# Optimization experiments

Measured on AMD Instinct MI355X. Metric: run time of the kernel, lower is better.

## Reference

```python
import jax, jax.numpy as jnp
import numpy as np

B_NW, N, DIM, NH, DH, HID, NW, WH = 2048, 64, 512, 16, 32, 384, 64, 8
EPS = 1e-12  # F.normalize eps

def _rel_coords_log(wh, ww):
    # torch.cartesian_prod order: i (rows) outer, j (cols) inner
    ii, jj = np.meshgrid(np.arange(wh), np.arange(ww), indexing='ij')
    coords = np.stack([ii.ravel(), jj.ravel()], axis=-1).astype(np.float32)  # [N,2]
    rel = coords[:, None, :] - coords[None, :, :]                            # [N,N,2]
    return (np.sign(rel) * np.log1p(np.abs(rel))).astype(np.float32)

def setup_inputs() -> dict:
    key = jax.random.key(0)
    ks = jax.random.split(key, 9)
    s = 0.02
    inner = NH * DH
    return {
        'x': jax.random.normal(ks[0], (B_NW, N, DIM), jnp.float32),
        'mask': jax.random.normal(ks[1], (NW, N, N), jnp.float32),
        'w_qkv': jax.random.normal(ks[2], (DIM, 3 * inner), jnp.float32) * s,
        'tau': jnp.ones((1, NH, 1, 1), jnp.float32),
        'mlp_w1': jax.random.normal(ks[3], (2, HID), jnp.float32) * s,
        'mlp_b1': jnp.zeros((HID,), jnp.float32),
        'mlp_w2': jax.random.normal(ks[4], (HID, NH), jnp.float32) * s,
        'mlp_b2': jnp.zeros((NH,), jnp.float32),
        'w_out': jax.random.normal(ks[5], (inner, DIM), jnp.float32) * s,
        'b_out': jnp.zeros((DIM,), jnp.float32),
        'rel_log': jnp.asarray(_rel_coords_log(WH, WH)),
    }

def reference(x, mask, w_qkv, tau, mlp_w1, mlp_b1, mlp_w2, mlp_b2, w_out, b_out, rel_log):
    b, n, _ = x.shape
    qkv = x @ w_qkv                                   # [b, n, 3*nh*dh]
    qkv = qkv.reshape(b, n, 3, NH, DH)
    q, k, v = (jnp.transpose(qkv[:, :, i], (0, 2, 1, 3)) for i in range(3))  # [b, nh, n, dh]
    # cosine attention: L2-normalize q and k along head dim
    q = q / jnp.maximum(jnp.linalg.norm(q, axis=-1, keepdims=True), EPS)
    k = k / jnp.maximum(jnp.linalg.norm(k, axis=-1, keepdims=True), EPS)
    sim = jnp.einsum('bhid,bhjd->bhij', q, k) * tau   # learned temperature
    # relative position bias via meta MLP: [N,N,2] -> [N,N,nh]
    bias = jax.nn.relu(rel_log @ mlp_w1 + mlp_b1) @ mlp_w2 + mlp_b2
    sim = sim + jnp.transpose(bias, (2, 0, 1))[None]  # [1, nh, N, N]
    nw = mask.shape[0]
    sim = sim.reshape(b // nw, nw, NH, n, n) + mask[None, :, None]
    sim = sim.reshape(b, NH, n, n)
    attn = jax.nn.softmax(sim, axis=-1)
    out = jnp.einsum('bhij,bhjd->bhid', attn, v)
    out = jnp.transpose(out, (0, 2, 1, 3)).reshape(b, n, NH * DH)
    return out @ w_out + b_out
```

## Files before the change

### kernel.cpp

```cpp
#include <hip/hip_runtime.h>
#include <hip/hip_bf16.h>


typedef __bf16 bf16;
typedef __bf16 v4bf __attribute__((ext_vector_type(4)));
typedef __bf16 v8bf __attribute__((ext_vector_type(8)));
typedef float  v4f  __attribute__((ext_vector_type(4)));

__device__ __forceinline__ int swz(int o) { return o ^ (((o >> 7) & 7) << 4); }

__global__ void convert_w_kernel(const float* __restrict__ wqkv, const float* __restrict__ wout,
                                 bf16* __restrict__ Wt, bf16* __restrict__ WoT) {
    int idx = blockIdx.x * 256 + threadIdx.x;
    Wt[idx] = (bf16)wqkv[(idx & 511) * 1536 + (idx >> 9)];
    if (idx < 262144) WoT[idx] = (bf16)wout[(idx & 511) * 512 + (idx >> 9)];
}

__global__ void bias_kernel(const float* __restrict__ rel_log, const float* __restrict__ w1,
                            const float* __restrict__ b1, const float* __restrict__ w2,
                            const float* __restrict__ b2, float* __restrict__ bias) {
    int p = blockIdx.x * 256 + threadIdx.x;
    float ra = rel_log[p * 2 + 0];
    float rb = rel_log[p * 2 + 1];
    float acc[16];
    #pragma unroll
    for (int t = 0; t < 16; ++t) acc[t] = 0.f;
    for (int kk = 0; kk < 384; ++kk) {
        float hv = fmaxf(ra * w1[kk] + rb * w1[384 + kk] + b1[kk], 0.f);
        #pragma unroll
        for (int t = 0; t < 16; ++t) acc[t] += hv * w2[kk * 16 + t];
    }
    #pragma unroll
    for (int t = 0; t < 16; ++t) bias[t * 4096 + p] = acc[t] + b2[t];
}

__global__ void comb_kernel(const float* __restrict__ bias, const float* __restrict__ mask,
                            float* __restrict__ comb) {
    int idx = blockIdx.x * 256 + threadIdx.x;
    int t = idx & 4095, wh = idx >> 12;
    int w = wh >> 4, h = wh & 15;
    int ji = t >> 8, rem = t & 255;
    int j = ji >> 2, i = ji & 3;
    int q16 = rem >> 2, r = t & 3;
    int lq = q16 >> 4, lm = q16 & 15;
    int p = (i * 16 + lm) * 64 + j * 16 + lq * 4 + r;
    comb[idx] = bias[h * 4096 + p] + mask[w * 4096 + p];
}

__global__ __launch_bounds__(256) void qkv_gemm_kernel(
    const float* __restrict__ x,
    const bf16* __restrict__ Wt,
    bf16* __restrict__ q_ws, bf16* __restrict__ k_ws, bf16* __restrict__ v_ws)
{
    __shared__ alignas(16) char Alds[2][8192];
    __shared__ alignas(16) char Blds[2][8192];
    const int bid = blockIdx.x, nwg = gridDim.x;
    const int wid = (bid & 7) * (nwg >> 3) + (bid >> 3);
    const int nb = wid % 12, mb = wid / 12;

    const int t = threadIdx.x;
    const int wv = t >> 6, lane = t & 63, lq = lane >> 4, lm = lane & 15;
    const int wr = wv >> 1, wc = wv & 1;

    const int srow = t >> 1, scol = (t & 1) * 16;
    const float* aptr = x + (size_t)(mb * 128 + srow) * 512 + scol;
    const int wbyte = srow * 64 + scol * 2;
    const int wo0 = swz(wbyte), wo1 = swz(wbyte + 16);

    const char* bBase = (const char*)Wt + (size_t)(nb * 128) * 1024;
    int so[2], brow[2], bcol[2];
    #pragma unroll
    for (int p = 0; p < 2; ++p) {
        so[p] = p * 4096 + t * 16;
        int s = swz(so[p]);
        brow[p] = s >> 6; bcol[p] = s & 63;
    }
    auto stageB = [&](int buf, int kt) {
        #pragma unroll
        for (int p = 0; p < 2; ++p)
            __builtin_amdgcn_global_load_lds(
                (const __attribute__((address_space(1))) void*)(bBase + (size_t)brow[p] * 1024 + kt * 64 + bcol[p]),
                (__attribute__((address_space(3))) void*)(&Blds[buf][0] + so[p]),
                16, 0, 0);
    };
    auto writeA = [&](int buf, float4 f0, float4 f1, float4 f2, float4 f3) {
        v8bf a0 = { (bf16)f0.x, (bf16)f0.y, (bf16)f0.z, (bf16)f0.w,
                    (bf16)f1.x, (bf16)f1.y, (bf16)f1.z, (bf16)f1.w };
        v8bf a1 = { (bf16)f2.x, (bf16)f2.y, (bf16)f2.z, (bf16)f2.w,
                    (bf16)f3.x, (bf16)f3.y, (bf16)f3.z, (bf16)f3.w };
        *(v8bf*)(&Alds[buf][0] + wo0) = a0;
        *(v8bf*)(&Alds[buf][0] + wo1) = a1;
    };

    int aoff[4], boff[4];
    #pragma unroll
    for (int i = 0; i < 4; ++i) {
        aoff[i] = swz((wr * 64 + i * 16 + lm) * 64 + lq * 16);
        boff[i] = swz((wc * 64 + i * 16 + lm) * 64 + lq * 16);
    }

    v4f acc[4][4];
    #pragma unroll
    for (int i = 0; i < 4; ++i)
        #pragma unroll
        for (int j = 0; j < 4; ++j) acc[i][j] = v4f{0.f, 0.f, 0.f, 0.f};

    {
        const float4* ap = (const float4*)aptr;
        float4 f0 = ap[0], f1 = ap[1], f2 = ap[2], f3 = ap[3];
        stageB(0, 0);
        writeA(0, f0, f1, f2, f3);
        __syncthreads();
    }

    #pragma unroll 1
    for (int kt = 0; kt < 16; ++kt) {
        const int cur = kt & 1;
        float4 f0, f1, f2, f3;
        if (kt < 15) {
            const float4* ap = (const float4*)(aptr + (kt + 1) * 32);
            f0 = ap[0]; f1 = ap[1]; f2 = ap[2]; f3 = ap[3];
            stageB(cur ^ 1, kt + 1);
        }
        v8bf af[4], bfj[4];
        #pragma unroll
        for (int i = 0; i < 4; ++i) af[i] = *(const v8bf*)(&Alds[cur][0] + aoff[i]);
        #pragma unroll
        for (int j = 0; j < 4; ++j) bfj[j] = *(const v8bf*)(&Blds[cur][0] + boff[j]);
        #pragma unroll
        for (int i = 0; i < 4; ++i)
            #pragma unroll
            for (int j = 0; j < 4; ++j)
                acc[i][j] = __builtin_amdgcn_mfma_f32_16x16x32_bf16(af[i], bfj[j], acc[i][j], 0, 0, 0);
        if (kt < 15) writeA(cur ^ 1, f0, f1, f2, f3);
        __syncthreads();
    }

    const int bw = mb * 2 + wr;
    if (nb < 8) {
        bf16* dst = (nb < 4) ? q_ws : k_ws;
        const int hbase = (nb & 3) * 4 + wc * 2;
        #pragma unroll
        for (int tpair = 0; tpair < 2; ++tpair) {
            const int h = hbase + tpair;
            #pragma unroll
            for (int i = 0; i < 4; ++i)
                #pragma unroll
                for (int r = 0; r < 4; ++r) {
                    int n = i * 16 + lq * 4 + r;
                    size_t base = ((size_t)(bw * 16 + h) * 64 + n) * 32;
                    dst[base + lm]      = (bf16)acc[i][2 * tpair][r];
                    dst[base + 16 + lm] = (bf16)acc[i][2 * tpair + 1][r];
                }
        }
    } else {
        #pragma unroll
        for (int j = 0; j < 4; ++j) {
            const int h = (nb - 8) * 4 + wc * 2 + (j >> 1);
            const int dh = (j & 1) * 16 + lm;
            #pragma unroll
            for (int i = 0; i < 4; ++i) {
                v4bf pv = { (bf16)acc[i][j][0], (bf16)acc[i][j][1],
                            (bf16)acc[i][j][2], (bf16)acc[i][j][3] };
                *(v4bf*)(v_ws + ((size_t)(bw * 16 + h) * 32 + dh) * 64 + i * 16 + lq * 4) = pv;
            }
        }
    }
}

__global__ __launch_bounds__(256) void attn_kernel(
    const bf16* __restrict__ q_ws,
    const bf16* __restrict__ k_ws,
    const bf16* __restrict__ v_ws,
    const float* __restrict__ comb,
    const float* __restrict__ tau,
    int wofs,
    bf16* __restrict__ attn_out)
{
    __shared__ alignas(16) bf16 P_all[4][64 * 72];
    const int blk = blockIdx.x;
    const int b = blk >> 2, g = blk & 3;
    const int tid = threadIdx.x;
    const int wv = tid >> 6, lane = tid & 63, lq = lane >> 4, lm = lane & 15;
    const int h = g * 4 + wv;
    const v4f z4 = {0.f, 0.f, 0.f, 0.f};

    bf16* P = P_all[wv];
    const size_t qk_base = (size_t)(b * 16 + h) * 64 * 32;
    const float* comb_hw = comb + ((size_t)(((wofs + b) & 63) * 16 + h)) * 4096
                                + (lq * 16 + lm) * 4;
    const float tau_h = tau[h];

    v8bf qf[4], kf[4];
    #pragma unroll
    for (int i = 0; i < 4; ++i)
        qf[i] = *(const v8bf*)(q_ws + qk_base + (i * 16 + lm) * 32 + lq * 8);
    #pragma unroll
    for (int j = 0; j < 4; ++j)
        kf[j] = *(const v8bf*)(k_ws + qk_base + (j * 16 + lm) * 32 + lq * 8);

    #pragma unroll
    for (int i = 0; i < 4; ++i) {
        float a = 0.f;
        #pragma unroll
        for (int e = 0; e < 8; ++e) { float f = (float)qf[i][e]; a = fmaf(f, f, a); }
        a += __shfl_xor(a, 16); a += __shfl_xor(a, 32);
        float sc = tau_h / fmaxf(sqrtf(a), 1e-12f);
        #pragma unroll
        for (int e = 0; e < 8; ++e) qf[i][e] = (bf16)((float)qf[i][e] * sc);
    }
    #pragma unroll
    for (int j = 0; j < 4; ++j) {
        float a = 0.f;
        #pragma unroll
        for (int e = 0; e < 8; ++e) { float f = (float)kf[j][e]; a = fmaf(f, f, a); }
        a += __shfl_xor(a, 16); a += __shfl_xor(a, 32);
        float sc = 1.0f / fmaxf(sqrtf(a), 1e-12f);
        #pragma unroll
        for (int e = 0; e < 8; ++e) kf[j][e] = (bf16)((float)kf[j][e] * sc);
    }

    v4f st[4][4];
    #pragma unroll
    for (int j = 0; j < 4; ++j)
        #pragma unroll
        for (int i = 0; i < 4; ++i)
            st[j][i] = __builtin_amdgcn_mfma_f32_16x16x32_bf16(kf[j], qf[i], z4, 0, 0, 0);

    #pragma unroll
    for (int j = 0; j < 4; ++j)
        #pragma unroll
        for (int i = 0; i < 4; ++i) {
            float4 cv = *(const float4*)(comb_hw + (j * 4 + i) * 256);
            st[j][i][0] += cv.x; st[j][i][1] += cv.y;
            st[j][i][2] += cv.z; st[j][i][3] += cv.w;
        }

    #pragma unroll
    for (int i = 0; i < 4; ++i) {
        float mx = st[0][i][0];
        #pragma unroll
        for (int j = 0; j < 4; ++j)
            #pragma unroll
            for (int r = 0; r < 4; ++r) mx = fmaxf(mx, st[j][i][r]);
        mx = fmaxf(mx, __shfl_xor(mx, 16));
        mx = fmaxf(mx, __shfl_xor(mx, 32));
        float sm = 0.f;
        #pragma unroll
        for (int j = 0; j < 4; ++j)
            #pragma unroll
            for (int r = 0; r < 4; ++r) {
                float e = __expf(st[j][i][r] - mx);
                st[j][i][r] = e; sm += e;
            }
        sm += __shfl_xor(sm, 16); sm += __shfl_xor(sm, 32);
        float rcp = 1.0f / sm;
        #pragma unroll
        for (int j = 0; j < 4; ++j) {
            v4bf pv = { (bf16)(st[j][i][0] * rcp), (bf16)(st[j][i][1] * rcp),
                        (bf16)(st[j][i][2] * rcp), (bf16)(st[j][i][3] * rcp) };
            *(v4bf*)(P + (i * 16 + lm) * 72 + j * 16 + lq * 4) = pv;
        }
    }

    const size_t v_base = (size_t)(b * 16 + h) * 32 * 64;
    v4f o[4][2];
    #pragma unroll
    for (int i = 0; i < 4; ++i)
        #pragma unroll
        for (int nt = 0; nt < 2; ++nt) o[i][nt] = z4;
    #pragma unroll
    for (int kk = 0; kk < 2; ++kk) {
        v8bf vf[2], pf[4];
        #pragma unroll
        for (int nt = 0; nt < 2; ++nt)
            vf[nt] = *(const v8bf*)(v_ws + v_base + (nt * 16 + lm) * 64 + kk * 32 + lq * 8);
        #pragma unroll
        for (int i = 0; i < 4; ++i)
            pf[i] = *(const v8bf*)(P + (i * 16 + lm) * 72 + kk * 32 + lq * 8);
        #pragma unroll
        for (int i = 0; i < 4; ++i)
            #pragma unroll
            for (int nt = 0; nt < 2; ++nt)
                o[i][nt] = __builtin_amdgcn_mfma_f32_16x16x32_bf16(pf[i], vf[nt], o[i][nt], 0, 0, 0);
    }
    #pragma unroll
    for (int i = 0; i < 4; ++i)
        #pragma unroll
        for (int nt = 0; nt < 2; ++nt)
            #pragma unroll
            for (int r = 0; r < 4; ++r)
                attn_out[(size_t)(b * 64 + i * 16 + lq * 4 + r) * 512 + h * 32 + nt * 16 + lm] =
                    (bf16)o[i][nt][r];
}

__global__ __launch_bounds__(256) void proj_gemm_kernel(
    const bf16* __restrict__ A,
    const bf16* __restrict__ Bt,
    const float* __restrict__ b_out,
    float* __restrict__ out)
{
    __shared__ alignas(16) bf16 Alds[2][128 * 32];
    __shared__ alignas(16) bf16 Blds[2][128 * 32];
    const int bid = blockIdx.x;
    const int wid = (bid & 7) * 512 + (bid >> 3);
    const int mb = wid >> 2, nb = wid & 3;
    const int tid = threadIdx.x;
    const int wv = tid >> 6, lane = tid & 63, lq = lane >> 4, lm = lane & 15;
    const int wr = wv >> 1, wc = wv & 1;

    const char* aBase = (const char*)A + (size_t)mb * 128 * 1024;
    const char* bBase = (const char*)Bt + (size_t)nb * 128 * 1024;

    auto stage = [&](int buf, int kt) {
        #pragma unroll
        for (int p = 0; p < 2; ++p) {
            int idx = (p * 4 + wv) * 1024 + lane * 16;
            int row = idx >> 6, kb = idx & 63;
            __builtin_amdgcn_global_load_lds(
                (const __attribute__((address_space(1))) void*)(aBase + (size_t)row * 1024 + kt * 64 + kb),
                (__attribute__((address_space(3))) void*)((char*)Alds + buf * 8192 + (p * 4 + wv) * 1024),
                16, 0, 0);
            __builtin_amdgcn_global_load_lds(
                (const __attribute__((address_space(1))) void*)(bBase + (size_t)row * 1024 + kt * 64 + kb),
                (__attribute__((address_space(3))) void*)((char*)Blds + buf * 8192 + (p * 4 + wv) * 1024),
                16, 0, 0);
        }
    };

    v4f acc[4][4];
    #pragma unroll
    for (int i = 0; i < 4; ++i)
        #pragma unroll
        for (int j = 0; j < 4; ++j) acc[i][j] = v4f{0.f, 0.f, 0.f, 0.f};

    stage(0, 0);
    #pragma unroll 1
    for (int kt = 0; kt < 16; ++kt) {
        if (kt < 15) {
            stage((kt + 1) & 1, kt + 1);
            asm volatile("s_waitcnt vmcnt(4)" ::: "memory");
        } else {
            asm volatile("s_waitcnt vmcnt(0)" ::: "memory");
        }
        __builtin_amdgcn_s_barrier();
        __builtin_amdgcn_sched_barrier(0);
        const bf16* Ab = &Alds[kt & 1][0];
        const bf16* Bb = &Blds[kt & 1][0];
        v8bf af[4], bfj[4];
        #pragma unroll
        for (int i = 0; i < 4; ++i)
            af[i] = *(const v8bf*)(Ab + (wr * 64 + i * 16 + lm) * 32 + lq * 8);
        #pragma unroll
        for (int j = 0; j < 4; ++j)
            bfj[j] = *(const v8bf*)(Bb + (wc * 64 + j * 16 + lm) * 32 + lq * 8);
        #pragma unroll
        for (int i = 0; i < 4; ++i)
            #pragma unroll
            for (int j = 0; j < 4; ++j)
                acc[i][j] = __builtin_amdgcn_mfma_f32_16x16x32_bf16(af[i], bfj[j], acc[i][j], 0, 0, 0);
        __builtin_amdgcn_s_barrier();
    }

    #pragma unroll
    for (int j = 0; j < 4; ++j) {
        int col = nb * 128 + wc * 64 + j * 16 + lm;
        float bo = b_out[col];
        #pragma unroll
        for (int i = 0; i < 4; ++i)
            #pragma unroll
            for (int r = 0; r < 4; ++r)
                out[(size_t)(mb * 128 + wr * 64 + i * 16 + lq * 4 + r) * 512 + col] = acc[i][j][r] + bo;
    }
}

extern "C" void kernel_launch(void* const* d_in, const int* in_sizes, int n_in,
                              void* d_out, int out_size, void* d_ws, size_t ws_size,
                              hipStream_t stream) {
    (void)in_sizes; (void)n_in; (void)out_size;
    const float* x       = (const float*)d_in[0];
    const float* mask    = (const float*)d_in[1];
    const float* w_qkv   = (const float*)d_in[2];
    const float* tau     = (const float*)d_in[3];
    const float* mlp_w1  = (const float*)d_in[4];
    const float* mlp_b1  = (const float*)d_in[5];
    const float* mlp_w2  = (const float*)d_in[6];
    const float* mlp_b2  = (const float*)d_in[7];
    const float* w_out   = (const float*)d_in[8];
    const float* b_out   = (const float*)d_in[9];
    const float* rel_log = (const float*)d_in[10];
    float* out = (float*)d_out;

    char* ws = (char*)d_ws;
    bf16*  Wt       = (bf16*)(ws);
    bf16*  WoT      = (bf16*)(ws + 1572864);
    float* bias     = (float*)(ws + 2097152);
    float* comb     = (float*)(ws + 2359296);
    bf16*  attn_out = (bf16*)(ws + 19136512);
    char*  qkv_base = ws + 153354240;

    size_t avail = (ws_size > 153354240ULL) ? ws_size - 153354240ULL : 0;
    int W = 2048;
    while (W > 128 && (size_t)W * 196608ULL > avail) W >>= 1;
    const size_t qkbuf = (size_t)W * 65536;
    bf16* qb = (bf16*)qkv_base;
    bf16* kb = (bf16*)(qkv_base + qkbuf);
    bf16* vb = (bf16*)(qkv_base + 2 * qkbuf);

    convert_w_kernel<<<3072, 256, 0, stream>>>(w_qkv, w_out, Wt, WoT);
    bias_kernel<<<16, 256, 0, stream>>>(rel_log, mlp_w1, mlp_b1, mlp_w2, mlp_b2, bias);
    comb_kernel<<<16384, 256, 0, stream>>>(bias, mask, comb);

    const int nchunk = 2048 / W;
    for (int c = 0; c < nchunk; ++c) {
        const float* xc = x + (size_t)c * W * 64 * 512;
        bf16* aoc = attn_out + (size_t)c * W * 64 * 512;
        qkv_gemm_kernel<<<6 * W, 256, 0, stream>>>(xc, Wt, qb, kb, vb);
        attn_kernel<<<4 * W, 256, 0, stream>>>(qb, kb, vb, comb, tau, c * W, aoc);
    }
    proj_gemm_kernel<<<4096, 256, 0, stream>>>(attn_out, WoT, b_out, out);
}
```

Measured before the change: 845.9 us.

## Stage fp32 activations directly into LDS via async loads in QKV GEMM

```diff
diff --git a/kernel.cpp b/kernel.cpp
--- a/kernel.cpp
+++ b/kernel.cpp
@@ -7,7 +7,7 @@
 typedef __bf16 v8bf __attribute__((ext_vector_type(8)));
 typedef float  v4f  __attribute__((ext_vector_type(4)));
 
-__device__ __forceinline__ int swz(int o) { return o ^ (((o >> 7) & 7) << 4); }
+__device__ __forceinline__ int swz32(int o) { return o ^ (((o >> 7) & 7) << 4); }
 
 __global__ void convert_w_kernel(const float* __restrict__ wqkv, const float* __restrict__ wout,
                                  bf16* __restrict__ Wt, bf16* __restrict__ WoT) {
@@ -52,7 +52,7 @@
     const bf16* __restrict__ Wt,
     bf16* __restrict__ q_ws, bf16* __restrict__ k_ws, bf16* __restrict__ v_ws)
 {
-    __shared__ alignas(16) char Alds[2][8192];
+    __shared__ alignas(16) char Alds[2][16384];
     __shared__ alignas(16) char Blds[2][8192];
     const int bid = blockIdx.x, nwg = gridDim.x;
     const int wid = (bid & 7) * (nwg >> 3) + (bid >> 3);
@@ -62,41 +62,40 @@
     const int wv = t >> 6, lane = t & 63, lq = lane >> 4, lm = lane & 15;
     const int wr = wv >> 1, wc = wv & 1;
 
-    const int srow = t >> 1, scol = (t & 1) * 16;
-    const float* aptr = x + (size_t)(mb * 128 + srow) * 512 + scol;
-    const int wbyte = srow * 64 + scol * 2;
-    const int wo0 = swz(wbyte), wo1 = swz(wbyte + 16);
-
+    const char* aBase = (const char*)x + (size_t)mb * 128 * 2048;
     const char* bBase = (const char*)Wt + (size_t)(nb * 128) * 1024;
-    int so[2], brow[2], bcol[2];
-    #pragma unroll
-    for (int p = 0; p < 2; ++p) {
-        so[p] = p * 4096 + t * 16;
-        int s = swz(so[p]);
-        brow[p] = s >> 6; bcol[p] = s & 63;
-    }
-    auto stageB = [&](int buf, int kt) {
-        #pragma unroll
-        for (int p = 0; p < 2; ++p)
+
+    int arow[4], acol[4];
+    #pragma unroll
+    for (int p = 0; p < 4; ++p) {
+        int s = swz32(p * 4096 + t * 16);
+        arow[p] = s >> 7; acol[p] = s & 127;
+    }
+    const int bo0 = t * 16, bo1 = 4096 + t * 16;
+    const int brow0 = bo0 >> 6, bcol0 = bo0 & 63;
+    const int brow1 = bo1 >> 6, bcol1 = bo1 & 63;
+
+    auto stage = [&](int buf, int kt) {
+        #pragma unroll
+        for (int p = 0; p < 4; ++p)
             __builtin_amdgcn_global_load_lds(
-                (const __attribute__((address_space(1))) void*)(bBase + (size_t)brow[p] * 1024 + kt * 64 + bcol[p]),
-                (__attribute__((address_space(3))) void*)(&Blds[buf][0] + so[p]),
+                (const __attribute__((address_space(1))) void*)(aBase + (size_t)arow[p] * 2048 + kt * 128 + acol[p]),
+                (__attribute__((address_space(3))) void*)(&Alds[buf][0] + p * 4096 + t * 16),
                 16, 0, 0);
+        __builtin_amdgcn_global_load_lds(
+            (const __attribute__((address_space(1))) void*)(bBase + (size_t)brow0 * 1024 + kt * 64 + bcol0),
+            (__attribute__((address_space(3))) void*)(&Blds[buf][0] + bo0), 16, 0, 0);
+        __builtin_amdgcn_global_load_lds(
+            (const __attribute__((address_space(1))) void*)(bBase + (size_t)brow1 * 1024 + kt * 64 + bcol1),
+            (__attribute__((address_space(3))) void*)(&Blds[buf][0] + bo1), 16, 0, 0);
     };
-    auto writeA = [&](int buf, float4 f0, float4 f1, float4 f2, float4 f3) {
-        v8bf a0 = { (bf16)f0.x, (bf16)f0.y, (bf16)f0.z, (bf16)f0.w,
-                    (bf16)f1.x, (bf16)f1.y, (bf16)f1.z, (bf16)f1.w };
-        v8bf a1 = { (bf16)f2.x, (bf16)f2.y, (bf16)f2.z, (bf16)f2.w,
-                    (bf16)f3.x, (bf16)f3.y, (bf16)f3.z, (bf16)f3.w };
-        *(v8bf*)(&Alds[buf][0] + wo0) = a0;
-        *(v8bf*)(&Alds[buf][0] + wo1) = a1;
-    };
 
     int aoff[4], boff[4];
     #pragma unroll
     for (int i = 0; i < 4; ++i) {
-        aoff[i] = swz((wr * 64 + i * 16 + lm) * 64 + lq * 16);
-        boff[i] = swz((wc * 64 + i * 16 + lm) * 64 + lq * 16);
+        int o0 = (wr * 64 + i * 16 + lm) * 128 + lq * 32;
+        aoff[i] = swz32(o0);
+        boff[i] = (wc * 64 + i * 16 + lm) * 64 + lq * 16;
     }
 
     v4f acc[4][4];
@@ -105,35 +104,36 @@
         #pragma unroll
         for (int j = 0; j < 4; ++j) acc[i][j] = v4f{0.f, 0.f, 0.f, 0.f};
 
-    {
-        const float4* ap = (const float4*)aptr;
-        float4 f0 = ap[0], f1 = ap[1], f2 = ap[2], f3 = ap[3];
-        stageB(0, 0);
-        writeA(0, f0, f1, f2, f3);
-        __syncthreads();
-    }
-
+    stage(0, 0);
     #pragma unroll 1
     for (int kt = 0; kt < 16; ++kt) {
-        const int cur = kt & 1;
-        float4 f0, f1, f2, f3;
         if (kt < 15) {
-            const float4* ap = (const float4*)(aptr + (kt + 1) * 32);
-            f0 = ap[0]; f1 = ap[1]; f2 = ap[2]; f3 = ap[3];
-            stageB(cur ^ 1, kt + 1);
-        }
+            stage((kt + 1) & 1, kt + 1);
+            asm volatile("s_waitcnt vmcnt(6)" ::: "memory");
+        } else {
+            asm volatile("s_waitcnt vmcnt(0)" ::: "memory");
+        }
+        __builtin_amdgcn_s_barrier();
+        __builtin_amdgcn_sched_barrier(0);
+        const char* Ab = &Alds[kt & 1][0];
+        const bf16* Bb = (const bf16*)&Blds[kt & 1][0];
         v8bf af[4], bfj[4];
         #pragma unroll
-        for (int i = 0; i < 4; ++i) af[i] = *(const v8bf*)(&Alds[cur][0] + aoff[i]);
-        #pragma unroll
-        for (int j = 0; j < 4; ++j) bfj[j] = *(const v8bf*)(&Blds[cur][0] + boff[j]);
+        for (int i = 0; i < 4; ++i) {
+            v4f lo = *(const v4f*)(Ab + aoff[i]);
+            v4f hi = *(const v4f*)(Ab + (aoff[i] ^ 16));
+            af[i] = v8bf{ (bf16)lo[0], (bf16)lo[1], (bf16)lo[2], (bf16)lo[3],
+                          (bf16)hi[0], (bf16)hi[1], (bf16)hi[2], (bf16)hi[3] };
+        }
+        #pragma unroll
+        for (int j = 0; j < 4; ++j)
+            bfj[j] = *(const v8bf*)(Bb + boff[j] / 2);
         #pragma unroll
         for (int i = 0; i < 4; ++i)
             #pragma unroll
             for (int j = 0; j < 4; ++j)
                 acc[i][j] = __builtin_amdgcn_mfma_f32_16x16x32_bf16(af[i], bfj[j], acc[i][j], 0, 0, 0);
-        if (kt < 15) writeA(cur ^ 1, f0, f1, f2, f3);
-        __syncthreads();
+        __builtin_amdgcn_s_barrier();
     }
 
     const int bw = mb * 2 + wr;
```

Result: faster. 753.7 us (-10.9%).
